# Kernel tuning notes

Measured on AMD Instinct MI355X. Metric: run time of the kernel, lower is better.

## Reference

```python
import jax, jax.numpy as jnp
import numpy as np

B, S, DMODEL, HEADS = 2, 2048, 1024, 16
DK = DMODEL // HEADS
DV = DMODEL // HEADS


def setup_inputs() -> dict:
    key = jax.random.key(0)
    kx, kq, kk, kv = jax.random.split(key, 4)
    x = jax.random.normal(kx, (B, S, DMODEL), dtype=jnp.float32)
    # stacked per-head projection weights, shape [H, dmodel, dk/dv]
    # (equivalent to nn.Linear(dmodel, dk, bias=False) per head)
    scale = 1.0 / np.sqrt(DMODEL)
    Wq = jax.random.uniform(kq, (HEADS, DMODEL, DK), jnp.float32, -scale, scale)
    Wk = jax.random.uniform(kk, (HEADS, DMODEL, DK), jnp.float32, -scale, scale)
    Wv = jax.random.uniform(kv, (HEADS, DMODEL, DV), jnp.float32, -scale, scale)
    return {"x": x, "Wq": Wq, "Wk": Wk, "Wv": Wv}


def reference(x, Wq, Wk, Wv):
    # per-head projections, batched across heads: [B,H,S,dk]
    q = jnp.einsum("bsd,hdk->bhsk", x, Wq)
    k = jnp.einsum("bsd,hdk->bhsk", x, Wk)
    v = jnp.einsum("bsd,hdv->bhsv", x, Wv)
    # NOTE: original module applies NO 1/sqrt(dk) scaling — keep faithful
    scores = jnp.einsum("bhqk,bhsk->bhqs", q, k)  # [B,H,S,S]
    attn = jax.nn.softmax(scores, axis=-1)
    out = jnp.einsum("bhqs,bhsv->bhqv", attn, v)  # [B,H,S,dv]
    # concat heads along last dim in head order
    Bsz, H, Sq, Dv = out.shape
    return jnp.transpose(out, (0, 2, 1, 3)).reshape(Bsz, Sq, H * Dv)
```

## Files before the change

### kernel.cpp

```cpp
#include <hip/hip_runtime.h>

#define B_ 2
#define S_ 2048
#define D_ 1024
#define H_ 16
#define DK_ 64
#define M_ (B_ * S_)
#define N_ (3 * D_)

typedef __bf16 bf16x8 __attribute__((ext_vector_type(8)));
typedef short s8vec __attribute__((ext_vector_type(8)));
typedef float f4vec __attribute__((ext_vector_type(4)));

static __device__ __forceinline__ ushort f2b(float f) {
  union { float f; unsigned u; } v; v.f = f;
  unsigned u = v.u;
  u += 0x7FFFu + ((u >> 16) & 1u);
  return (ushort)(u >> 16);
}

static __device__ __forceinline__ unsigned pk2(float a, float b) {
#if __has_builtin(__builtin_amdgcn_cvt_pk_bf16_f32)
  typedef __bf16 b2 __attribute__((ext_vector_type(2)));
  b2 r = __builtin_amdgcn_cvt_pk_bf16_f32(a, b);
  return __builtin_bit_cast(unsigned, r);
#else
  return (unsigned)f2b(a) | ((unsigned)f2b(b) << 16);
#endif
}

static __device__ __forceinline__ float exp2f_fast(float x) {
#if __has_builtin(__builtin_amdgcn_exp2f)
  return __builtin_amdgcn_exp2f(x);
#else
  return __expf(x * 0.6931471805599453f);
#endif
}

static __device__ __forceinline__ f4vec mfma16(s8vec a, s8vec b, f4vec c) {
  return __builtin_amdgcn_mfma_f32_16x16x32_bf16(
      __builtin_bit_cast(bf16x8, a), __builtin_bit_cast(bf16x8, b), c, 0, 0, 0);
}

static __device__ __forceinline__ void gl_lds16(const ushort* g, ushort* l) {
  __builtin_amdgcn_global_load_lds(
      (const __attribute__((address_space(1))) unsigned*)g,
      (__attribute__((address_space(3))) unsigned*)l, 16, 0, 0);
}

static __device__ __forceinline__ void wg_barrier_lds() {
  asm volatile("" ::: "memory");
  __builtin_amdgcn_s_waitcnt(0xC07F);
  __builtin_amdgcn_s_barrier();
  asm volatile("" ::: "memory");
}

__global__ void cvt_x(const float* __restrict__ x, ushort* __restrict__ xb) {
  int i = blockIdx.x * 256 + threadIdx.x;
  float4 v = ((const float4*)x)[i];
  ushort4 o;
  o.x = f2b(v.x); o.y = f2b(v.y); o.z = f2b(v.z); o.w = f2b(v.w);
  ((ushort4*)xb)[i] = o;
}

__global__ __launch_bounds__(256) void cvt_w(const float* __restrict__ Wq,
                                             const float* __restrict__ Wk,
                                             const float* __restrict__ Wv,
                                             ushort* __restrict__ wbt) {
  __shared__ ushort T[64 * 72];
  const int w = blockIdx.z, h = blockIdx.y, d0 = blockIdx.x * 64;
  const float* W = (w == 0) ? Wq : (w == 1) ? Wk : Wv;
  const float sc = (w == 0) ? 1.4426950408889634f : 1.0f;
  const float* src = W + (size_t)h * 65536 + (size_t)d0 * 64;
  const int t = threadIdx.x;
#pragma unroll
  for (int j = 0; j < 4; ++j) {
    int idx = j * 256 + t;
    int dr = idx >> 4, kc = (idx & 15) * 4;
    float4 v = *(const float4*)(src + dr * 64 + kc);
    T[(kc + 0) * 72 + dr] = f2b(v.x * sc);
    T[(kc + 1) * 72 + dr] = f2b(v.y * sc);
    T[(kc + 2) * 72 + dr] = f2b(v.z * sc);
    T[(kc + 3) * 72 + dr] = f2b(v.w * sc);
  }
  __syncthreads();
  const int kk = t >> 2, dcg = (t & 3) * 16;
  ushort* dst = wbt + ((size_t)w * 1024 + h * 64 + kk) * 1024 + d0 + dcg;
  *(s8vec*)dst       = *(const s8vec*)&T[kk * 72 + dcg];
  *(s8vec*)(dst + 8) = *(const s8vec*)&T[kk * 72 + dcg + 8];
}

__global__ __launch_bounds__(256) void proj_gemm(const ushort* __restrict__ xb,
                                                 const ushort* __restrict__ wbt,
                                                 ushort* __restrict__ qkv) {
  __shared__ __attribute__((aligned(16))) ushort As[128 * 64];
  __shared__ __attribute__((aligned(16))) ushort Bs[128 * 64];
  const int tid = threadIdx.x, wid = tid >> 6, lane = tid & 63;
  const int quad = lane >> 4, l15 = lane & 15;
  const int wm = wid & 1, wn = wid >> 1;
  const int m0 = blockIdx.x * 128, n0 = blockIdx.y * 128;

  f4vec acc[4][4];
#pragma unroll
  for (int mb = 0; mb < 4; mb++)
#pragma unroll
    for (int nb = 0; nb < 4; nb++)
#pragma unroll
      for (int i = 0; i < 4; i++) acc[mb][nb][i] = 0.f;

  const int sr = tid >> 3, sg = tid & 7;
  const int lg = sg ^ (sr & 7);
  const ushort* Ab = xb + (size_t)m0 * D_;
  const ushort* Bb = wbt + (size_t)n0 * D_;

  for (int k0 = 0; k0 < D_; k0 += 64) {
    __syncthreads();
#pragma unroll
    for (int j = 0; j < 4; ++j) {
      int r = j * 32 + sr;
      gl_lds16(Ab + (size_t)r * D_ + k0 + lg * 8, &As[j * 2048 + wid * 512]);
      gl_lds16(Bb + (size_t)r * D_ + k0 + lg * 8, &Bs[j * 2048 + wid * 512]);
    }
    __syncthreads();

#pragma unroll
    for (int kb = 0; kb < 2; ++kb) {
      s8vec af[4], bf[4];
#pragma unroll
      for (int mb = 0; mb < 4; ++mb) {
        int m = wm * 64 + mb * 16 + l15;
        int gpos = (kb * 4 + quad) ^ (m & 7);
        af[mb] = *(const s8vec*)&As[m * 64 + gpos * 8];
      }
#pragma unroll
      for (int nb = 0; nb < 4; ++nb) {
        int n = wn * 64 + nb * 16 + l15;
        int gpos = (kb * 4 + quad) ^ (n & 7);
        bf[nb] = *(const s8vec*)&Bs[n * 64 + gpos * 8];
      }
#pragma unroll
      for (int mb = 0; mb < 4; ++mb)
#pragma unroll
        for (int nb = 0; nb < 4; ++nb)
          acc[mb][nb] = mfma16(af[mb], bf[nb], acc[mb][nb]);
    }
  }

  const size_t per = (size_t)B_ * H_ * S_ * DK_;
  const int w = n0 >> 10;
  if (w == 2) {
    ushort* vt = qkv + 2 * per;
#pragma unroll
    for (int mb = 0; mb < 4; ++mb)
#pragma unroll
      for (int nb = 0; nb < 4; ++nb)
#pragma unroll
        for (int i = 0; i < 4; ++i) {
          int m = m0 + wm * 64 + mb * 16 + quad * 4 + i;
          int b = m >> 11, s = m & 2047;
          int n1 = (n0 & 1023) + wn * 64 + nb * 16 + l15;
          vt[((size_t)b * 1024 + n1) * S_ + s] = f2b(acc[mb][nb][i]);
        }
  } else {
#pragma unroll
    for (int mb = 0; mb < 4; ++mb)
#pragma unroll
      for (int nb = 0; nb < 4; ++nb)
#pragma unroll
        for (int i = 0; i < 4; ++i) {
          int m = m0 + wm * 64 + mb * 16 + quad * 4 + i;
          int b = m >> 11, s = m & 2047;
          int n1 = (n0 & 1023) + wn * 64 + nb * 16 + l15;
          qkv[(size_t)w * per + (((size_t)b * H_ + (n1 >> 6)) * S_ + s) * 64 + (n1 & 63)] =
              f2b(acc[mb][nb][i]);
        }
  }
}

__global__ __launch_bounds__(256) void attn(const ushort* __restrict__ qg,
                                            const ushort* __restrict__ kg,
                                            const ushort* __restrict__ vtg,
                                            float* __restrict__ out) {
  __shared__ __attribute__((aligned(16))) ushort Ks[128 * 64];
  __shared__ __attribute__((aligned(16))) ushort Vt[2][64 * 64];
  const int qt = blockIdx.x, bh = blockIdx.y;
  const int b = bh >> 4, h = bh & 15;
  const int tid = threadIdx.x, wid = tid >> 6, lane = tid & 63;
  const int quad = lane >> 4, l15 = lane & 15, l7 = l15 & 7;

  const ushort* qbase = qg + ((size_t)bh * S_ + qt * 128 + wid * 32) * DK_;
  s8vec bq[2][2];
#pragma unroll
  for (int qb = 0; qb < 2; ++qb)
#pragma unroll
    for (int kc = 0; kc < 2; ++kc)
      bq[qb][kc] = *(const s8vec*)(qbase + (size_t)(qb * 16 + l15) * DK_ + kc * 32 + quad * 8);

  f4vec o[4][2];
  float lsum[2] = {0.f, 0.f};
#pragma unroll
  for (int nb = 0; nb < 4; ++nb)
#pragma unroll
    for (int qb = 0; qb < 2; ++qb)
#pragma unroll
      for (int i = 0; i < 4; ++i) o[nb][qb][i] = 0.f;

  const int r5 = tid >> 3, gs = tid & 7;
  const int gk = gs ^ (r5 & 7);
  const ushort* kb_ = kg + (size_t)bh * S_ * DK_;
  const ushort* vb_ = vtg + (size_t)bh * 64 * S_;

  s8vec kr[4], vr[4];
#pragma unroll
  for (int j = 0; j < 4; ++j)
    kr[j] = *(const s8vec*)(kb_ + (size_t)(j * 32 + r5) * DK_ + gk * 8);
#pragma unroll
  for (int jd = 0; jd < 2; ++jd)
#pragma unroll
    for (int hf = 0; hf < 2; ++hf)
      vr[jd * 2 + hf] = *(const s8vec*)(vb_ + (size_t)(jd * 32 + r5) * S_ + hf * 64 + gk * 8);

  for (int kt = 0; kt < S_ / 128; ++kt) {
    wg_barrier_lds();
#pragma unroll
    for (int j = 0; j < 4; ++j)
      *(s8vec*)&Ks[(j * 32 + r5) * 64 + gs * 8] = kr[j];
#pragma unroll
    for (int jd = 0; jd < 2; ++jd)
#pragma unroll
      for (int hf = 0; hf < 2; ++hf)
        *(s8vec*)&Vt[hf][(jd * 32 + r5) * 64 + gs * 8] = vr[jd * 2 + hf];
    if (kt + 1 < S_ / 128) {
      const ushort* kn = kb_ + (size_t)(kt + 1) * 128 * DK_;
#pragma unroll
      for (int j = 0; j < 4; ++j)
        kr[j] = *(const s8vec*)(kn + (size_t)(j * 32 + r5) * DK_ + gk * 8);
      const ushort* vn = vb_ + (kt + 1) * 128;
#pragma unroll
      for (int jd = 0; jd < 2; ++jd)
#pragma unroll
        for (int hf = 0; hf < 2; ++hf)
          vr[jd * 2 + hf] = *(const s8vec*)(vn + (size_t)(jd * 32 + r5) * S_ + hf * 64 + gk * 8);
    }
    wg_barrier_lds();

#pragma unroll
    for (int kc2 = 0; kc2 < 4; ++kc2) {
      s8vec ak[2][2];
#pragma unroll
      for (int kbs = 0; kbs < 2; ++kbs) {
        const int row = (kc2 * 2 + kbs) * 16 + l15;
        ak[kbs][0] = *(const s8vec*)&Ks[row * 64 + ((0 + quad) ^ l7) * 8];
        ak[kbs][1] = *(const s8vec*)&Ks[row * 64 + ((4 + quad) ^ l7) * 8];
      }
      const int half = kc2 >> 1, G = (kc2 & 1) * 4 + quad;
      s8vec av[4];
#pragma unroll
      for (int nb = 0; nb < 4; ++nb)
        av[nb] = *(const s8vec*)&Vt[half][(nb * 16 + l15) * 64 + ((G) ^ l7) * 8];

      f4vec st[2][2];
#pragma unroll
      for (int kbs = 0; kbs < 2; ++kbs)
#pragma unroll
        for (int qb = 0; qb < 2; ++qb) {
          f4vec z;
#pragma unroll
          for (int i = 0; i < 4; ++i) z[i] = 0.f;
          z = mfma16(ak[kbs][0], bq[qb][0], z);
          st[kbs][qb] = mfma16(ak[kbs][1], bq[qb][1], z);
        }

#pragma unroll
      for (int qb = 0; qb < 2; ++qb) {
        float p0 = exp2f_fast(st[0][qb][0]), p1 = exp2f_fast(st[0][qb][1]);
        float p2 = exp2f_fast(st[0][qb][2]), p3 = exp2f_fast(st[0][qb][3]);
        float p4 = exp2f_fast(st[1][qb][0]), p5 = exp2f_fast(st[1][qb][1]);
        float p6 = exp2f_fast(st[1][qb][2]), p7 = exp2f_fast(st[1][qb][3]);
        lsum[qb] += ((p0 + p1) + (p2 + p3)) + ((p4 + p5) + (p6 + p7));
        unsigned w0 = pk2(p0, p1), w1 = pk2(p2, p3);
        unsigned w2 = pk2(p4, p5), w3 = pk2(p6, p7);
        asm("v_permlane32_swap_b32 %0, %1" : "+v"(w0), "+v"(w2));
        asm("v_permlane16_swap_b32 %0, %1" : "+v"(w0), "+v"(w2));
        asm("v_permlane32_swap_b32 %0, %1" : "+v"(w1), "+v"(w3));
        asm("v_permlane16_swap_b32 %0, %1" : "+v"(w1), "+v"(w3));
        union { unsigned u[4]; s8vec v; } pb;
        pb.u[0] = w0; pb.u[1] = w1; pb.u[2] = w2; pb.u[3] = w3;
#pragma unroll
        for (int nb = 0; nb < 4; ++nb) o[nb][qb] = mfma16(av[nb], pb.v, o[nb][qb]);
      }
    }
  }

  float inv[2];
#pragma unroll
  for (int qb = 0; qb < 2; ++qb) {
    float s = lsum[qb];
    s += __shfl_xor(s, 16, 64);
    s += __shfl_xor(s, 32, 64);
    inv[qb] = 1.0f / s;
  }

  float* ob = out + ((size_t)b * S_ + qt * 128 + wid * 32) * D_ + h * DK_;
#pragma unroll
  for (int qb = 0; qb < 2; ++qb)
#pragma unroll
    for (int nb = 0; nb < 4; ++nb) {
      float4 vvv;
      vvv.x = o[nb][qb][0] * inv[qb];
      vvv.y = o[nb][qb][1] * inv[qb];
      vvv.z = o[nb][qb][2] * inv[qb];
      vvv.w = o[nb][qb][3] * inv[qb];
      *(float4*)&ob[(size_t)(qb * 16 + l15) * D_ + nb * 16 + quad * 4] = vvv;
    }
}

extern "C" void kernel_launch(void* const* d_in, const int* in_sizes, int n_in,
                              void* d_out, int out_size, void* d_ws, size_t ws_size,
                              hipStream_t stream) {
  const float* x  = (const float*)d_in[0];
  const float* Wq = (const float*)d_in[1];
  const float* Wk = (const float*)d_in[2];
  const float* Wv = (const float*)d_in[3];
  float* out = (float*)d_out;

  ushort* xb  = (ushort*)d_ws;
  ushort* wbt = xb + (size_t)B_ * S_ * D_;
  ushort* qkv = wbt + (size_t)3 * D_ * D_;
  const size_t per = (size_t)B_ * H_ * S_ * DK_;

  cvt_x<<<(B_ * S_ * D_) / 4 / 256, 256, 0, stream>>>(x, xb);
  cvt_w<<<dim3(16, 16, 3), 256, 0, stream>>>(Wq, Wk, Wv, wbt);
  proj_gemm<<<dim3(M_ / 128, N_ / 128), 256, 0, stream>>>(xb, wbt, qkv);
  attn<<<dim3(S_ / 128, B_ * H_), 256, 0, stream>>>(qkv, qkv + per, qkv + 2 * per, out);
}
```

Before: 172.9 us.

## Split attention over key dimension, add merge kernel, fuse conversion kernels

Splits the key loop of the attention kernel into two halves launched on a third grid dimension, which doubles the block count from 512 to 1024 so the GPU has more parallel work. Each half writes an unnormalized partial output and row sums, and a new merge kernel adds the halves and normalizes. The split avoids a running max because the scores are never max-shifted. It also fuses the x and W conversion kernels into one launch, adds s_setprio around the MFMA sections, and sets a launch-bounds occupancy hint. The cost is an extra kernel launch plus extra global traffic for the partial outputs and row sums.

```diff
diff --git a/kernel.cpp b/kernel.cpp
--- a/kernel.cpp
+++ b/kernel.cpp
@@ -7,6 +7,8 @@
 #define DK_ 64
 #define M_ (B_ * S_)
 #define N_ (3 * D_)
+#define KSPLIT 2
+#define NT_ (S_ / 128 / KSPLIT)
 
 typedef __bf16 bf16x8 __attribute__((ext_vector_type(8)));
 typedef short s8vec __attribute__((ext_vector_type(8)));
@@ -55,24 +57,27 @@
   asm volatile("" ::: "memory");
 }
 
-__global__ void cvt_x(const float* __restrict__ x, ushort* __restrict__ xb) {
-  int i = blockIdx.x * 256 + threadIdx.x;
-  float4 v = ((const float4*)x)[i];
-  ushort4 o;
-  o.x = f2b(v.x); o.y = f2b(v.y); o.z = f2b(v.z); o.w = f2b(v.w);
-  ((ushort4*)xb)[i] = o;
-}
-
-__global__ __launch_bounds__(256) void cvt_w(const float* __restrict__ Wq,
-                                             const float* __restrict__ Wk,
-                                             const float* __restrict__ Wv,
-                                             ushort* __restrict__ wbt) {
+__global__ __launch_bounds__(256) void cvt_xw(const float* __restrict__ x,
+                                              const float* __restrict__ Wq,
+                                              const float* __restrict__ Wk,
+                                              const float* __restrict__ Wv,
+                                              ushort* __restrict__ xb,
+                                              ushort* __restrict__ wbt) {
   __shared__ ushort T[64 * 72];
-  const int w = blockIdx.z, h = blockIdx.y, d0 = blockIdx.x * 64;
+  const int t = threadIdx.x;
+  if (blockIdx.x < 4096) {
+    int i = blockIdx.x * 256 + t;
+    float4 v = ((const float4*)x)[i];
+    ushort4 o;
+    o.x = f2b(v.x); o.y = f2b(v.y); o.z = f2b(v.z); o.w = f2b(v.w);
+    ((ushort4*)xb)[i] = o;
+    return;
+  }
+  const int r = blockIdx.x - 4096;
+  const int w = r >> 8, h = (r >> 4) & 15, d0 = (r & 15) * 64;
   const float* W = (w == 0) ? Wq : (w == 1) ? Wk : Wv;
   const float sc = (w == 0) ? 1.4426950408889634f : 1.0f;
   const float* src = W + (size_t)h * 65536 + (size_t)d0 * 64;
-  const int t = threadIdx.x;
 #pragma unroll
   for (int j = 0; j < 4; ++j) {
     int idx = j * 256 + t;
@@ -177,14 +182,17 @@
   }
 }
 
-__global__ __launch_bounds__(256) void attn(const ushort* __restrict__ qg,
-                                            const ushort* __restrict__ kg,
-                                            const ushort* __restrict__ vtg,
-                                            float* __restrict__ out) {
+__global__ __launch_bounds__(256, 4) void attn(const ushort* __restrict__ qg,
+                                               const ushort* __restrict__ kg,
+                                               const ushort* __restrict__ vtg,
+                                               float* __restrict__ out,
+                                               float* __restrict__ op1,
+                                               float* __restrict__ ls) {
   __shared__ __attribute__((aligned(16))) ushort Ks[128 * 64];
   __shared__ __attribute__((aligned(16))) ushort Vt[2][64 * 64];
-  const int qt = blockIdx.x, bh = blockIdx.y;
+  const int qt = blockIdx.x, bh = blockIdx.y, z = blockIdx.z;
   const int b = bh >> 4, h = bh & 15;
+  const int kt0 = z * NT_;
   const int tid = threadIdx.x, wid = tid >> 6, lane = tid & 63;
   const int quad = lane >> 4, l15 = lane & 15, l7 = l15 & 7;
 
@@ -213,14 +221,15 @@
   s8vec kr[4], vr[4];
 #pragma unroll
   for (int j = 0; j < 4; ++j)
-    kr[j] = *(const s8vec*)(kb_ + (size_t)(j * 32 + r5) * DK_ + gk * 8);
+    kr[j] = *(const s8vec*)(kb_ + (size_t)(kt0 * 128 + j * 32 + r5) * DK_ + gk * 8);
 #pragma unroll
   for (int jd = 0; jd < 2; ++jd)
 #pragma unroll
     for (int hf = 0; hf < 2; ++hf)
-      vr[jd * 2 + hf] = *(const s8vec*)(vb_ + (size_t)(jd * 32 + r5) * S_ + hf * 64 + gk * 8);
-
-  for (int kt = 0; kt < S_ / 128; ++kt) {
+      vr[jd * 2 + hf] =
+          *(const s8vec*)(vb_ + (size_t)(jd * 32 + r5) * S_ + kt0 * 128 + hf * 64 + gk * 8);
+
+  for (int kt = kt0; kt < kt0 + NT_; ++kt) {
     wg_barrier_lds();
 #pragma unroll
     for (int j = 0; j < 4; ++j)
@@ -230,7 +239,7 @@
 #pragma unroll
       for (int hf = 0; hf < 2; ++hf)
         *(s8vec*)&Vt[hf][(jd * 32 + r5) * 64 + gs * 8] = vr[jd * 2 + hf];
-    if (kt + 1 < S_ / 128) {
+    if (kt + 1 < kt0 + NT_) {
       const ushort* kn = kb_ + (size_t)(kt + 1) * 128 * DK_;
 #pragma unroll
       for (int j = 0; j < 4; ++j)
@@ -257,19 +266,21 @@
       s8vec av[4];
 #pragma unroll
       for (int nb = 0; nb < 4; ++nb)
-        av[nb] = *(const s8vec*)&Vt[half][(nb * 16 + l15) * 64 + ((G) ^ l7) * 8];
+        av[nb] = *(const s8vec*)&Vt[half][(nb * 16 + l15) * 64 + (G ^ l7) * 8];
 
       f4vec st[2][2];
+      __builtin_amdgcn_s_setprio(1);
 #pragma unroll
       for (int kbs = 0; kbs < 2; ++kbs)
 #pragma unroll
         for (int qb = 0; qb < 2; ++qb) {
-          f4vec z;
-#pragma unroll
-          for (int i = 0; i < 4; ++i) z[i] = 0.f;
-          z = mfma16(ak[kbs][0], bq[qb][0], z);
-          st[kbs][qb] = mfma16(ak[kbs][1], bq[qb][1], z);
+          f4vec zz;
+#pragma unroll
+          for (int i = 0; i < 4; ++i) zz[i] = 0.f;
+          zz = mfma16(ak[kbs][0], bq[qb][0], zz);
+          st[kbs][qb] = mfma16(ak[kbs][1], bq[qb][1], zz);
         }
+      __builtin_amdgcn_s_setprio(0);
 
 #pragma unroll
       for (int qb = 0; qb < 2; ++qb) {
@@ -286,33 +297,73 @@
         asm("v_permlane16_swap_b32 %0, %1" : "+v"(w1), "+v"(w3));
         union { unsigned u[4]; s8vec v; } pb;
         pb.u[0] = w0; pb.u[1] = w1; pb.u[2] = w2; pb.u[3] = w3;
+        __builtin_amdgcn_s_setprio(1);
 #pragma unroll
         for (int nb = 0; nb < 4; ++nb) o[nb][qb] = mfma16(av[nb], pb.v, o[nb][qb]);
+        __builtin_amdgcn_s_setprio(0);
       }
     }
   }
 
-  float inv[2];
+  float lrow[2];
 #pragma unroll
   for (int qb = 0; qb < 2; ++qb) {
     float s = lsum[qb];
     s += __shfl_xor(s, 16, 64);
     s += __shfl_xor(s, 32, 64);
-    inv[qb] = 1.0f / s;
-  }
-
-  float* ob = out + ((size_t)b * S_ + qt * 128 + wid * 32) * D_ + h * DK_;
-#pragma unroll
-  for (int qb = 0; qb < 2; ++qb)
-#pragma unroll
-    for (int nb = 0; nb < 4; ++nb) {
-      float4 vvv;
-      vvv.x = o[nb][qb][0] * inv[qb];
-      vvv.y = o[nb][qb][1] * inv[qb];
-      vvv.z = o[nb][qb][2] * inv[qb];
-      vvv.w = o[nb][qb][3] * inv[qb];
-      *(float4*)&ob[(size_t)(qb * 16 + l15) * D_ + nb * 16 + quad * 4] = vvv;
-    }
+    lrow[qb] = s;
+  }
+  if (lane < 16) {
+#pragma unroll
+    for (int qb = 0; qb < 2; ++qb)
+      ls[(size_t)z * (B_ * H_ * S_) + (size_t)bh * S_ + qt * 128 + wid * 32 + qb * 16 + l15] =
+          lrow[qb];
+  }
+
+  if (z == 0) {
+    float* ob = out + ((size_t)b * S_ + qt * 128 + wid * 32) * D_ + h * DK_;
+#pragma unroll
+    for (int qb = 0; qb < 2; ++qb)
+#pragma unroll
+      for (int nb = 0; nb < 4; ++nb) {
+        float4 vvv;
+        vvv.x = o[nb][qb][0]; vvv.y = o[nb][qb][1];
+        vvv.z = o[nb][qb][2]; vvv.w = o[nb][qb][3];
+        *(float4*)&ob[(size_t)(qb * 16 + l15) * D_ + nb * 16 + quad * 4] = vvv;
+      }
+  } else {
+    float* ob = op1 + ((size_t)bh * S_ + qt * 128 + wid * 32) * 64;
+#pragma unroll
+    for (int qb = 0; qb < 2; ++qb)
+#pragma unroll
+      for (int nb = 0; nb < 4; ++nb) {
+        float4 vvv;
+        vvv.x = o[nb][qb][0]; vvv.y = o[nb][qb][1];
+        vvv.z = o[nb][qb][2]; vvv.w = o[nb][qb][3];
+        *(float4*)&ob[(size_t)(qb * 16 + l15) * 64 + nb * 16 + quad * 4] = vvv;
+      }
+  }
+}
+
+__global__ __launch_bounds__(256) void merge(float* __restrict__ out,
+                                             const float* __restrict__ op1,
+                                             const float* __restrict__ ls) {
+  const int i = blockIdx.x * 256 + threadIdx.x;
+  const int e = i * 4;
+  const int d = e & (D_ - 1);
+  const int s = (e >> 10) & (S_ - 1);
+  const int b = e >> 21;
+  const int bh = b * H_ + (d >> 6);
+  const size_t row = (size_t)bh * S_ + s;
+  const float l = ls[row] + ls[(size_t)(B_ * H_ * S_) + row];
+  const float inv = 1.0f / l;
+  float4 a = ((const float4*)out)[i];
+  float4 c = ((const float4*)op1)[row * 16 + ((d & 63) >> 2)];
+  a.x = (a.x + c.x) * inv;
+  a.y = (a.y + c.y) * inv;
+  a.z = (a.z + c.z) * inv;
+  a.w = (a.w + c.w) * inv;
+  ((float4*)out)[i] = a;
 }
 
 extern "C" void kernel_launch(void* const* d_in, const int* in_sizes, int n_in,
@@ -328,9 +379,12 @@
   ushort* wbt = xb + (size_t)B_ * S_ * D_;
   ushort* qkv = wbt + (size_t)3 * D_ * D_;
   const size_t per = (size_t)B_ * H_ * S_ * DK_;
-
-  cvt_x<<<(B_ * S_ * D_) / 4 / 256, 256, 0, stream>>>(x, xb);
-  cvt_w<<<dim3(16, 16, 3), 256, 0, stream>>>(Wq, Wk, Wv, wbt);
+  float* ls  = (float*)(qkv + 3 * per);
+  float* op1 = ls + (size_t)2 * B_ * H_ * S_;
+
+  cvt_xw<<<4096 + 768, 256, 0, stream>>>(x, Wq, Wk, Wv, xb, wbt);
   proj_gemm<<<dim3(M_ / 128, N_ / 128), 256, 0, stream>>>(xb, wbt, qkv);
-  attn<<<dim3(S_ / 128, B_ * H_), 256, 0, stream>>>(qkv, qkv + per, qkv + 2 * per, out);
-}
+  attn<<<dim3(S_ / 128, B_ * H_, KSPLIT), 256, 0, stream>>>(qkv, qkv + per, qkv + 2 * per,
+                                                            out, op1, ls);
+  merge<<<(B_ * S_ * D_) / 4 / 256, 256, 0, stream>>>(out, op1, ls);
+}
```

Result: slower. 312.2 us (+80.6%).

## Software-pipeline attention inner loop and merge input conversion kernels

Applied to the files above, without the earlier changes.

The attention tile loop is restructured so the QK^T MFMAs for the next 32-key chunk are issued before the softmax and PV MFMAs of the current chunk. K fragments are double-buffered and V fragments are loaded one step ahead. The aim is to hide LDS read latency and the gap between the two MFMA stages behind the exp and permlane work. Separately, the x and weight bf16 conversion kernels are merged into one launch, indexed by blockIdx, to save one launch. The cost is higher register pressure from the extra buffered fragments and score tiles.

```diff
diff --git a/kernel.cpp b/kernel.cpp
--- a/kernel.cpp
+++ b/kernel.cpp
@@ -55,24 +55,27 @@
   asm volatile("" ::: "memory");
 }
 
-__global__ void cvt_x(const float* __restrict__ x, ushort* __restrict__ xb) {
-  int i = blockIdx.x * 256 + threadIdx.x;
-  float4 v = ((const float4*)x)[i];
-  ushort4 o;
-  o.x = f2b(v.x); o.y = f2b(v.y); o.z = f2b(v.z); o.w = f2b(v.w);
-  ((ushort4*)xb)[i] = o;
-}
-
-__global__ __launch_bounds__(256) void cvt_w(const float* __restrict__ Wq,
-                                             const float* __restrict__ Wk,
-                                             const float* __restrict__ Wv,
-                                             ushort* __restrict__ wbt) {
+__global__ __launch_bounds__(256) void cvt_xw(const float* __restrict__ x,
+                                              const float* __restrict__ Wq,
+                                              const float* __restrict__ Wk,
+                                              const float* __restrict__ Wv,
+                                              ushort* __restrict__ xb,
+                                              ushort* __restrict__ wbt) {
   __shared__ ushort T[64 * 72];
-  const int w = blockIdx.z, h = blockIdx.y, d0 = blockIdx.x * 64;
+  const int t = threadIdx.x;
+  if (blockIdx.x < 4096) {
+    int i = blockIdx.x * 256 + t;
+    float4 v = ((const float4*)x)[i];
+    ushort4 o;
+    o.x = f2b(v.x); o.y = f2b(v.y); o.z = f2b(v.z); o.w = f2b(v.w);
+    ((ushort4*)xb)[i] = o;
+    return;
+  }
+  const int r = blockIdx.x - 4096;
+  const int w = r >> 8, h = (r >> 4) & 15, d0 = (r & 15) * 64;
   const float* W = (w == 0) ? Wq : (w == 1) ? Wk : Wv;
   const float sc = (w == 0) ? 1.4426950408889634f : 1.0f;
   const float* src = W + (size_t)h * 65536 + (size_t)d0 * 64;
-  const int t = threadIdx.x;
 #pragma unroll
   for (int j = 0; j < 4; ++j) {
     int idx = j * 256 + t;
@@ -220,6 +223,64 @@
     for (int hf = 0; hf < 2; ++hf)
       vr[jd * 2 + hf] = *(const s8vec*)(vb_ + (size_t)(jd * 32 + r5) * S_ + hf * 64 + gk * 8);
 
+#define LDAK(i, buf)                                                      \
+  do {                                                                    \
+    const int r0_ = ((i) * 2 + 0) * 16 + l15;                             \
+    const int r1_ = ((i) * 2 + 1) * 16 + l15;                             \
+    akb[buf][0] = *(const s8vec*)&Ks[r0_ * 64 + ((0 + quad) ^ l7) * 8];   \
+    akb[buf][1] = *(const s8vec*)&Ks[r0_ * 64 + ((4 + quad) ^ l7) * 8];   \
+    akb[buf][2] = *(const s8vec*)&Ks[r1_ * 64 + ((0 + quad) ^ l7) * 8];   \
+    akb[buf][3] = *(const s8vec*)&Ks[r1_ * 64 + ((4 + quad) ^ l7) * 8];   \
+  } while (0)
+
+#define LDAV(i)                                                           \
+  do {                                                                    \
+    const int hf_ = (i) >> 1, G_ = ((i) & 1) * 4 + quad;                  \
+    _Pragma("unroll")                                                     \
+    for (int nb = 0; nb < 4; ++nb)                                        \
+      avb[nb] = *(const s8vec*)&Vt[hf_][(nb * 16 + l15) * 64 + (G_ ^ l7) * 8]; \
+  } while (0)
+
+#define QKC(buf)                                                          \
+  do {                                                                    \
+    _Pragma("unroll")                                                     \
+    for (int kbs = 0; kbs < 2; ++kbs)                                     \
+      _Pragma("unroll")                                                   \
+      for (int qb = 0; qb < 2; ++qb) {                                    \
+        f4vec zz;                                                         \
+        zz[0] = zz[1] = zz[2] = zz[3] = 0.f;                              \
+        zz = mfma16(akb[buf][kbs * 2 + 0], bq[qb][0], zz);                \
+        stb[buf][kbs][qb] = mfma16(akb[buf][kbs * 2 + 1], bq[qb][1], zz); \
+      }                                                                   \
+  } while (0)
+
+#define SMPV(buf)                                                         \
+  do {                                                                    \
+    _Pragma("unroll")                                                     \
+    for (int qb = 0; qb < 2; ++qb) {                                      \
+      float p0 = exp2f_fast(stb[buf][0][qb][0]);                          \
+      float p1 = exp2f_fast(stb[buf][0][qb][1]);                          \
+      float p2 = exp2f_fast(stb[buf][0][qb][2]);                          \
+      float p3 = exp2f_fast(stb[buf][0][qb][3]);                          \
+      float p4 = exp2f_fast(stb[buf][1][qb][0]);                          \
+      float p5 = exp2f_fast(stb[buf][1][qb][1]);                          \
+      float p6 = exp2f_fast(stb[buf][1][qb][2]);                          \
+      float p7 = exp2f_fast(stb[buf][1][qb][3]);                          \
+      lsum[qb] += ((p0 + p1) + (p2 + p3)) + ((p4 + p5) + (p6 + p7));      \
+      unsigned w0 = pk2(p0, p1), w1 = pk2(p2, p3);                        \
+      unsigned w2 = pk2(p4, p5), w3 = pk2(p6, p7);                        \
+      asm("v_permlane32_swap_b32 %0, %1" : "+v"(w0), "+v"(w2));           \
+      asm("v_permlane16_swap_b32 %0, %1" : "+v"(w0), "+v"(w2));           \
+      asm("v_permlane32_swap_b32 %0, %1" : "+v"(w1), "+v"(w3));           \
+      asm("v_permlane16_swap_b32 %0, %1" : "+v"(w1), "+v"(w3));           \
+      union { unsigned u[4]; s8vec v; } pb;                               \
+      pb.u[0] = w0; pb.u[1] = w1; pb.u[2] = w2; pb.u[3] = w3;             \
+      _Pragma("unroll")                                                   \
+      for (int nb = 0; nb < 4; ++nb)                                      \
+        o[nb][qb] = mfma16(avb[nb], pb.v, o[nb][qb]);                     \
+    }                                                                     \
+  } while (0)
+
   for (int kt = 0; kt < S_ / 128; ++kt) {
     wg_barrier_lds();
 #pragma unroll
@@ -244,53 +305,27 @@
     }
     wg_barrier_lds();
 
-#pragma unroll
-    for (int kc2 = 0; kc2 < 4; ++kc2) {
-      s8vec ak[2][2];
-#pragma unroll
-      for (int kbs = 0; kbs < 2; ++kbs) {
-        const int row = (kc2 * 2 + kbs) * 16 + l15;
-        ak[kbs][0] = *(const s8vec*)&Ks[row * 64 + ((0 + quad) ^ l7) * 8];
-        ak[kbs][1] = *(const s8vec*)&Ks[row * 64 + ((4 + quad) ^ l7) * 8];
-      }
-      const int half = kc2 >> 1, G = (kc2 & 1) * 4 + quad;
-      s8vec av[4];
-#pragma unroll
-      for (int nb = 0; nb < 4; ++nb)
-        av[nb] = *(const s8vec*)&Vt[half][(nb * 16 + l15) * 64 + ((G) ^ l7) * 8];
-
-      f4vec st[2][2];
-#pragma unroll
-      for (int kbs = 0; kbs < 2; ++kbs)
-#pragma unroll
-        for (int qb = 0; qb < 2; ++qb) {
-          f4vec z;
-#pragma unroll
-          for (int i = 0; i < 4; ++i) z[i] = 0.f;
-          z = mfma16(ak[kbs][0], bq[qb][0], z);
-          st[kbs][qb] = mfma16(ak[kbs][1], bq[qb][1], z);
-        }
-
-#pragma unroll
-      for (int qb = 0; qb < 2; ++qb) {
-        float p0 = exp2f_fast(st[0][qb][0]), p1 = exp2f_fast(st[0][qb][1]);
-        float p2 = exp2f_fast(st[0][qb][2]), p3 = exp2f_fast(st[0][qb][3]);
-        float p4 = exp2f_fast(st[1][qb][0]), p5 = exp2f_fast(st[1][qb][1]);
-        float p6 = exp2f_fast(st[1][qb][2]), p7 = exp2f_fast(st[1][qb][3]);
-        lsum[qb] += ((p0 + p1) + (p2 + p3)) + ((p4 + p5) + (p6 + p7));
-        unsigned w0 = pk2(p0, p1), w1 = pk2(p2, p3);
-        unsigned w2 = pk2(p4, p5), w3 = pk2(p6, p7);
-        asm("v_permlane32_swap_b32 %0, %1" : "+v"(w0), "+v"(w2));
-        asm("v_permlane16_swap_b32 %0, %1" : "+v"(w0), "+v"(w2));
-        asm("v_permlane32_swap_b32 %0, %1" : "+v"(w1), "+v"(w3));
-        asm("v_permlane16_swap_b32 %0, %1" : "+v"(w1), "+v"(w3));
-        union { unsigned u[4]; s8vec v; } pb;
-        pb.u[0] = w0; pb.u[1] = w1; pb.u[2] = w2; pb.u[3] = w3;
-#pragma unroll
-        for (int nb = 0; nb < 4; ++nb) o[nb][qb] = mfma16(av[nb], pb.v, o[nb][qb]);
-      }
-    }
-  }
+    s8vec akb[2][4];
+    s8vec avb[4];
+    f4vec stb[2][2][2];
+
+    LDAK(0, 0);
+    LDAV(0);
+    LDAK(1, 1);
+    QKC(0);
+#pragma unroll
+    for (int i = 0; i < 4; ++i) {
+      const int cur = i & 1, nxt = cur ^ 1;
+      if (i < 2) LDAK(i + 2, cur);
+      if (i < 3) QKC(nxt);
+      SMPV(cur);
+      if (i < 3) LDAV(i + 1);
+    }
+  }
+#undef LDAK
+#undef LDAV
+#undef QKC
+#undef SMPV
 
   float inv[2];
 #pragma unroll
@@ -329,8 +364,7 @@
   ushort* qkv = wbt + (size_t)3 * D_ * D_;
   const size_t per = (size_t)B_ * H_ * S_ * DK_;
 
-  cvt_x<<<(B_ * S_ * D_) / 4 / 256, 256, 0, stream>>>(x, xb);
-  cvt_w<<<dim3(16, 16, 3), 256, 0, stream>>>(Wq, Wk, Wv, wbt);
+  cvt_xw<<<4096 + 768, 256, 0, stream>>>(x, Wq, Wk, Wv, xb, wbt);
   proj_gemm<<<dim3(M_ / 128, N_ / 128), 256, 0, stream>>>(xb, wbt, qkv);
   attn<<<dim3(S_ / 128, B_ * H_), 256, 0, stream>>>(qkv, qkv + per, qkv + 2 * per, out);
 }
```

Result: no change. 174.8 us (+1.1%).
